# Kernel tuning notes

Measured on AMD Instinct MI355X. Metric: run time of the kernel, lower is better.

## Reference

```python
import jax, jax.numpy as jnp
import numpy as np


def _conv1x1(x, w, b=None):
    # x: (N,C,H,W), w: (O,C) -> (N,O,H,W)
    y = jnp.einsum('nchw,oc->nohw', x, w)
    return y if b is None else y + b[None, :, None, None]


def _norm(f):
    # per-channel zero-mean / unit-std over (N,H,W); torch.std is unbiased (ddof=1)
    mean = f.mean(axis=(0, 2, 3), keepdims=True)
    std = f.std(axis=(0, 2, 3), ddof=1, keepdims=True)
    return (f - mean) / (std + 1e-6)


def _causal_attention(x, w_cls):
    N, C, H, W = x.shape
    M = _conv1x1(x, w_cls).reshape(N, -1, H * W)     # (N,K,HW)
    sm = jax.nn.softmax(M, axis=2)                   # softmax over spatial
    return jnp.einsum('nkp,ncp->nkc', sm, x.reshape(N, C, H * W))  # (N,K,C)


def _ccnet(x, wq, bq, wk, bk, wv, bv, gamma1):
    B, C, H, W = x.shape
    q = _conv1x1(x, wq, bq)  # (B,Cq,H,W)
    k = _conv1x1(x, wk, bk)
    v = _conv1x1(x, wv, bv)  # (B,C,H,W)
    # column (vertical) attention energies with -inf on the self diagonal
    eH = jnp.einsum('bciw,bcjw->biwj', q, k)         # (B,H,W,H)
    eH = jnp.where(jnp.eye(H, dtype=bool)[None, :, None, :], -jnp.inf, eH)
    # row (horizontal) attention energies
    eW = jnp.einsum('bchi,bchj->bhij', q, k)         # (B,H,W,W)
    att = jax.nn.softmax(jnp.concatenate([eH, eW], axis=3), axis=3)
    attH, attW = att[..., :H], att[..., H:]
    outH = jnp.einsum('bcjw,biwj->bciw', v, attH)    # aggregate along column
    outW = jnp.einsum('bchj,bhij->bchi', v, attW)    # aggregate along row
    return gamma1 * (outH + outW) + x


def setup_inputs() -> dict:
    key = jax.random.key(0)
    ks = jax.random.split(key, 10)
    B, C, H, W = 8, 256, 96, 96
    Cq, K = C // 8, 6
    f32 = jnp.float32
    return {
        'preds_S': jax.random.normal(ks[0], (B, C, H, W), f32),
        'preds_T': jax.random.normal(ks[1], (B, C, H, W), f32),
        'w_cls': jax.random.normal(ks[2], (K, C), f32) * 0.05,
        'wq': jax.random.normal(ks[3], (Cq, C), f32) * 0.05,
        'bq': jnp.zeros((Cq,), f32),
        'wk': jax.random.normal(ks[4], (Cq, C), f32) * 0.05,
        'bk': jnp.zeros((Cq,), f32),
        'wv': jax.random.normal(ks[5], (C, C), f32) * 0.05,
        'bv': jnp.zeros((C,), f32),
        'gamma1': jax.random.normal(ks[6], (1,), f32) * 0.1,
    }


def reference(preds_S, preds_T, w_cls, wq, bq, wk, bk, wv, bv, gamma1):
    CA_W, CC_W = 0.0005, 1e-05
    N = preds_S.shape[0]
    s = _norm(preds_S)
    t = _norm(preds_T)
    ca_t = _causal_attention(t, w_cls)
    ca_s = _causal_attention(s, w_cls)
    ca_loss = jnp.sum((ca_t - ca_s) ** 2) / N
    cc_t = _ccnet(t, wq, bq, wk, bk, wv, bv, gamma1)
    cc_s = _ccnet(s, wq, bq, wk, bk, wv, bv, gamma1)
    cc_loss = jnp.sum((cc_t - cc_s) ** 2) / N
    return ca_loss * CA_W + cc_loss * CC_W
```

## Files before the change

### kernel.cpp

```cpp
#include <hip/hip_runtime.h>
#include <math.h>

#define NBAT 8
#define NC   256
#define NH   96
#define NW   96
#define NP   9216
#define NCQ  32
#define NKC  6
#define NL   192
#define NV   320
#define NTOT 73728

typedef __attribute__((ext_vector_type(4))) float  floatx4;
typedef __attribute__((ext_vector_type(8))) short  short8;

__device__ __forceinline__ float bf2f(unsigned short h){
  return __uint_as_float(((unsigned)h) << 16);
}
__device__ __forceinline__ unsigned short f2bf(float f){
  unsigned u = __float_as_uint(f);
  u += 0x7FFFu + ((u >> 16) & 1u);
  return (unsigned short)(u >> 16);
}

union F4 { float4 v; float a[4]; };

__device__ __forceinline__ float warpReduceSum(float v){
  #pragma unroll
  for (int m = 32; m; m >>= 1) v += __shfl_xor(v, m);
  return v;
}
__device__ __forceinline__ float warpReduceMax(float v){
  #pragma unroll
  for (int m = 32; m; m >>= 1) v = fmaxf(v, __shfl_xor(v, m));
  return v;
}
__device__ float blockReduceSum(float v){
  __shared__ float lds[8];
  v = warpReduceSum(v);
  int wid = threadIdx.x >> 6, lane = threadIdx.x & 63;
  int nw = blockDim.x >> 6;
  if (lane == 0) lds[wid] = v;
  __syncthreads();
  if (wid == 0){
    v = (lane < nw) ? lds[lane] : 0.f;
    #pragma unroll
    for (int m = 4; m; m >>= 1) v += __shfl_xor(v, m);
  }
  __syncthreads();
  return v;
}
__device__ float blockReduceMax(float v){
  __shared__ float lds[8];
  v = warpReduceMax(v);
  int wid = threadIdx.x >> 6, lane = threadIdx.x & 63;
  int nw = blockDim.x >> 6;
  if (lane == 0) lds[wid] = v;
  __syncthreads();
  if (wid == 0){
    v = (lane < nw) ? lds[lane] : -INFINITY;
    #pragma unroll
    for (int m = 4; m; m >>= 1) v = fmaxf(v, __shfl_xor(v, m));
  }
  __syncthreads();
  return v;
}

__global__ __launch_bounds__(256)
void k_stats(const float* __restrict__ S, const float* __restrict__ T,
             float* __restrict__ s_sum, float* __restrict__ s_sq){
  int blk = blockIdx.x;
  int t = blk / (NC * NBAT);
  int rem = blk % (NC * NBAT);
  int c = rem / NBAT;
  int n = rem % NBAT;
  const float4* x4 = (const float4*)((t ? T : S) + ((size_t)n * NC + c) * NP);
  float s = 0.f, q = 0.f;
  for (int p = threadIdx.x; p < NP / 4; p += 256){
    F4 f; f.v = x4[p];
    #pragma unroll
    for (int j = 0; j < 4; j++){ s += f.a[j]; q += f.a[j] * f.a[j]; }
  }
  s = blockReduceSum(s);
  q = blockReduceSum(q);
  if (threadIdx.x == 0){
    atomicAdd(&s_sum[t * NC + c], s);
    atomicAdd(&s_sq[t * NC + c], q);
  }
}

__global__ __launch_bounds__(512)
void k_finalize(const float* __restrict__ s_sum, const float* __restrict__ s_sq,
                float* __restrict__ mean, float* __restrict__ inv){
  int i = threadIdx.x;
  if (i < 2 * NC){
    float s = s_sum[i], q = s_sq[i];
    float m = s / (float)NTOT;
    float var = (q - s * m) / (float)(NTOT - 1);
    var = fmaxf(var, 0.f);
    mean[i] = m;
    inv[i] = 1.f / (sqrtf(var) + 1e-6f);
  }
}

__global__ __launch_bounds__(256)
void k_xn(const float* __restrict__ S, const float* __restrict__ T, int b0,
          const float* __restrict__ mean, const float* __restrict__ inv,
          unsigned short* __restrict__ XNT, unsigned short* __restrict__ XNS){
  int pt = blockIdx.x, ct = blockIdx.y;
  int bb = blockIdx.z >> 1, ts = blockIdx.z & 1;
  int t = ts ? 0 : 1;
  const float* x0 = ts ? S : T;
  unsigned short* XN = (ts ? XNS : XNT) + (size_t)bb * NP * NC;
  int bg = b0 + bb;
  int p0 = pt * 64, c0 = ct * 64;
  __shared__ float tile[64 * 65];
  const float* x = x0 + ((size_t)bg * NC + c0) * NP + p0;
  #pragma unroll
  for (int i = 0; i < 4; i++){
    int idx = threadIdx.x + i * 256;
    int r = idx >> 4, g = (idx & 15) * 4;
    F4 f; f.v = *(const float4*)(x + (size_t)r * NP + g);
    float m = mean[t * NC + c0 + r], iv = inv[t * NC + c0 + r];
    #pragma unroll
    for (int j = 0; j < 4; j++) tile[(g + j) * 65 + r] = (f.a[j] - m) * iv;
  }
  __syncthreads();
  #pragma unroll
  for (int i = 0; i < 4; i++){
    int idx = threadIdx.x + i * 256;
    int p = idx >> 4, g = (idx & 15) * 4;
    unsigned lo = (unsigned)f2bf(tile[p * 65 + g + 0]) | ((unsigned)f2bf(tile[p * 65 + g + 1]) << 16);
    unsigned hi = (unsigned)f2bf(tile[p * 65 + g + 2]) | ((unsigned)f2bf(tile[p * 65 + g + 3]) << 16);
    uint2 u; u.x = lo; u.y = hi;
    *(uint2*)(XN + ((size_t)(p0 + p)) * NC + c0 + g) = u;
  }
}

__global__ __launch_bounds__(256)
void k_caM(const unsigned short* __restrict__ XNT, const unsigned short* __restrict__ XNS,
           const float* __restrict__ wcls, int b0,
           float* __restrict__ smca){
  int pt = blockIdx.x, bb = blockIdx.y, ts = blockIdx.z;
  int t = ts ? 0 : 1;
  const unsigned short* XN = (ts ? XNS : XNT) + (size_t)bb * NP * NC;
  __shared__ float wcf[NKC * NC];
  for (int idx = threadIdx.x; idx < NKC * NC; idx += 256) wcf[idx] = wcls[idx];
  __syncthreads();
  int p = pt * 256 + threadIdx.x;
  const unsigned short* row = XN + (size_t)p * NC;
  float acc[NKC];
  #pragma unroll
  for (int k = 0; k < NKC; k++) acc[k] = 0.f;
  for (int c = 0; c < NC; c += 8){
    short8 v = *(const short8*)(row + c);
    #pragma unroll
    for (int j = 0; j < 8; j++){
      float xv = bf2f((unsigned short)v[j]);
      #pragma unroll
      for (int k = 0; k < NKC; k++) acc[k] += wcf[k * NC + c + j] * xv;
    }
  }
  size_t base = ((size_t)(t * NBAT + b0 + bb) * NKC) * NP + p;
  #pragma unroll
  for (int k = 0; k < NKC; k++) smca[base + (size_t)k * NP] = acc[k];
}

__global__ __launch_bounds__(256)
void k_caSoftmax(float* __restrict__ smca, int b0){
  int r = blockIdx.x;
  int bb = r / (2 * NKC);
  int rem = r % (2 * NKC);
  int ts = rem / NKC, k = rem % NKC;
  int t = ts ? 0 : 1;
  float* row = smca + ((size_t)(t * NBAT + b0 + bb) * NKC + k) * NP;
  float m = -INFINITY;
  for (int p = threadIdx.x; p < NP; p += 256) m = fmaxf(m, row[p]);
  m = blockReduceMax(m);
  __shared__ float bm, bs;
  if (threadIdx.x == 0) bm = m;
  __syncthreads();
  m = bm;
  float s = 0.f;
  for (int p = threadIdx.x; p < NP; p += 256) s += expf(row[p] - m);
  s = blockReduceSum(s);
  if (threadIdx.x == 0) bs = 1.f / s;
  __syncthreads();
  float rs = bs;
  for (int p = threadIdx.x; p < NP; p += 256) row[p] = expf(row[p] - m) * rs;
}

__global__ __launch_bounds__(256)
void k_caOut(const unsigned short* __restrict__ XNT, const unsigned short* __restrict__ XNS,
             const float* __restrict__ smca, int b0,
             float* __restrict__ ca){
  int ks = blockIdx.x, bb = blockIdx.y, ts = blockIdx.z;
  int t = ts ? 0 : 1;
  const unsigned short* XN = (ts ? XNS : XNT) + (size_t)bb * NP * NC;
  int p0 = ks * 256;
  __shared__ float smt[NKC * 256];
  const float* smbase = smca + (size_t)(t * NBAT + b0 + bb) * NKC * NP;
  for (int idx = threadIdx.x; idx < NKC * 256; idx += 256){
    int k = idx >> 8, pp = idx & 255;
    smt[idx] = smbase[(size_t)k * NP + p0 + pp];
  }
  __syncthreads();
  int c = threadIdx.x;
  float acc[NKC];
  #pragma unroll
  for (int k = 0; k < NKC; k++) acc[k] = 0.f;
  const unsigned short* xp = XN + (size_t)p0 * NC + c;
  for (int pp = 0; pp < 256; pp++){
    float xv = bf2f(xp[(size_t)pp * NC]);
    #pragma unroll
    for (int k = 0; k < NKC; k++) acc[k] += smt[k * 256 + pp] * xv;
  }
  float* cab = ca + ((size_t)(t * NBAT + b0 + bb) * NKC) * NC + c;
  #pragma unroll
  for (int k = 0; k < NKC; k++) atomicAdd(&cab[(size_t)k * NC], acc[k]);
}

__global__ __launch_bounds__(256)
void k_caLoss(const float* __restrict__ ca, float* __restrict__ out){
  int i = blockIdx.x * 256 + threadIdx.x;
  float d = 0.f;
  if (i < NBAT * NKC * NC) d = ca[(size_t)NBAT * NKC * NC + i] - ca[i];
  float ss = blockReduceSum(d * d);
  if (threadIdx.x == 0) atomicAdd(out, ss * (0.0005f / 8.0f));
}

__global__ __launch_bounds__(256)
void k_wconv(const float* __restrict__ wv, const float* __restrict__ wq,
             const float* __restrict__ wk, unsigned short* __restrict__ Wb){
  int n = blockIdx.x;
  const float* src = (n < 256) ? (wv + (size_t)n * NC)
                   : (n < 288) ? (wq + (size_t)(n - 256) * NC)
                               : (wk + (size_t)(n - 288) * NC);
  Wb[(size_t)n * NC + threadIdx.x] = f2bf(src[threadIdx.x]);
}

__global__ __launch_bounds__(256)
void k_v(const unsigned short* __restrict__ XNT, const unsigned short* __restrict__ XNS,
         const unsigned short* __restrict__ Wb,
         const float* __restrict__ bv, const float* __restrict__ bq,
         const float* __restrict__ bk,
         unsigned short* __restrict__ VT1T, unsigned short* __restrict__ VT1S,
         unsigned short* __restrict__ qT, unsigned short* __restrict__ kT,
         unsigned short* __restrict__ qS, unsigned short* __restrict__ kS){
  int pt = blockIdx.x;
  int bb = blockIdx.y >> 1, ts = blockIdx.y & 1;
  const unsigned short* XN = (ts ? XNS : XNT) + (size_t)bb * NP * NC;
  unsigned short* VT1 = (ts ? VT1S : VT1T) + (size_t)bb * NP * NC;
  unsigned short* qb  = (ts ? qS : qT) + (size_t)bb * NP * NCQ;
  unsigned short* kb  = (ts ? kS : kT) + (size_t)bb * NP * NCQ;
  int p0 = pt * 64;
  __shared__ unsigned short Wl[NV * 40];
  int lane = threadIdx.x & 63;
  int wid = threadIdx.x >> 6;
  int col = lane & 15, quad = lane >> 4;
  const unsigned short* xnb = XN + (size_t)(p0 + wid * 16 + col) * NC;
  floatx4 acc[20];
  #pragma unroll
  for (int nt = 0; nt < 20; nt++) acc[nt] = (floatx4){0.f, 0.f, 0.f, 0.f};

  int ci_n[5], ci_k8[5];
  #pragma unroll
  for (int i = 0; i < 5; i++){ int ci = i * 256 + threadIdx.x; ci_n[i] = ci >> 2; ci_k8[i] = (ci & 3) * 8; }

  short8 w[5];
  #pragma unroll
  for (int i = 0; i < 5; i++)
    w[i] = *(const short8*)(Wb + (size_t)ci_n[i] * NC + ci_k8[i]);

  for (int ks = 0; ks < 8; ks++){
    if (ks) __syncthreads();
    #pragma unroll
    for (int i = 0; i < 5; i++)
      *(short8*)(Wl + ci_n[i] * 40 + ci_k8[i]) = w[i];
    __syncthreads();
    if (ks < 7){
      int k0n = (ks + 1) * 32;
      #pragma unroll
      for (int i = 0; i < 5; i++)
        w[i] = *(const short8*)(Wb + (size_t)ci_n[i] * NC + k0n + ci_k8[i]);
    }
    short8 a = *(const short8*)(xnb + ks * 32 + quad * 8);
    #pragma unroll
    for (int nt = 0; nt < 20; nt++){
      short8 b = *(const short8*)(Wl + (nt * 16 + col) * 40 + quad * 8);
      acc[nt] = __builtin_amdgcn_mfma_f32_16x16x32_bf16(a, b, acc[nt], 0, 0, 0);
    }
  }

  int prow0 = p0 + wid * 16 + quad * 4;
  #pragma unroll
  for (int nt = 0; nt < 16; nt++){
    int c = nt * 16 + col;
    float bias = bv[c];
    uint2 u;
    u.x = (unsigned)f2bf(acc[nt][0] + bias) | ((unsigned)f2bf(acc[nt][1] + bias) << 16);
    u.y = (unsigned)f2bf(acc[nt][2] + bias) | ((unsigned)f2bf(acc[nt][3] + bias) << 16);
    *(uint2*)(VT1 + (size_t)c * NP + prow0) = u;
  }
  #pragma unroll
  for (int nt = 16; nt < 18; nt++){
    int c = (nt - 16) * 16 + col;
    float bias = bq[c];
    #pragma unroll
    for (int i = 0; i < 4; i++)
      qb[((size_t)(prow0 + i)) * NCQ + c] = f2bf(acc[nt][i] + bias);
  }
  #pragma unroll
  for (int nt = 18; nt < 20; nt++){
    int c = (nt - 18) * 16 + col;
    float bias = bk[c];
    #pragma unroll
    for (int i = 0; i < 4; i++)
      kb[((size_t)(prow0 + i)) * NCQ + c] = f2bf(acc[nt][i] + bias);
  }
}

__global__ __launch_bounds__(256)
void k_vt(const unsigned short* __restrict__ VT1T, const unsigned short* __restrict__ VT1S,
          unsigned short* __restrict__ VT2T, unsigned short* __restrict__ VT2S){
  int c = blockIdx.x;
  int bb = blockIdx.y >> 1, ts = blockIdx.y & 1;
  const unsigned short* VT1 = (ts ? VT1S : VT1T) + (size_t)bb * NP * NC;
  unsigned short* VT2 = (ts ? VT2S : VT2T) + (size_t)bb * NP * NC;
  __shared__ unsigned short tile[96 * 104];
  size_t base = (size_t)c * NP;
  for (int idx = threadIdx.x; idx < 1152; idx += 256){
    int h = idx / 12, g = idx % 12;
    short8 v = *(const short8*)(VT1 + base + h * 96 + g * 8);
    #pragma unroll
    for (int kk = 0; kk < 8; kk++) tile[(g * 8 + kk) * 104 + h] = ((unsigned short*)&v)[kk];
  }
  __syncthreads();
  for (int idx = threadIdx.x; idx < 1152; idx += 256){
    int w = idx / 12, g = idx % 12;
    short8 v = *(const short8*)(tile + w * 104 + g * 8);
    *(short8*)(VT2 + base + w * 96 + g * 8) = v;
  }
}

__global__ __launch_bounds__(256)
void k_e(const unsigned short* __restrict__ qT, const unsigned short* __restrict__ kT,
         const unsigned short* __restrict__ qS, const unsigned short* __restrict__ kS,
         unsigned short* __restrict__ attT, unsigned short* __restrict__ attS){
  int x = blockIdx.x, which = blockIdx.z;
  int bb = blockIdx.y >> 1, ts = blockIdx.y & 1;
  const unsigned short* qb = (ts ? qS : qT) + (size_t)bb * NP * NCQ;
  const unsigned short* kb = (ts ? kS : kT) + (size_t)bb * NP * NCQ;
  unsigned short* att = (ts ? attS : attT) + (size_t)bb * NP * NL;
  int lane = threadIdx.x & 63, wid = threadIdx.x >> 6;
  int col = lane & 15, quad = lane >> 4;
  int mi0 = (wid & 1) * 3, ni0 = (wid >> 1) * 3;
  short8 a[3], b[3];
  if (which == 0){
    #pragma unroll
    for (int m = 0; m < 3; m++)
      a[m] = *(const short8*)(qb + ((size_t)(((mi0 + m) * 16 + col) * 96 + x)) * NCQ + quad * 8);
    #pragma unroll
    for (int n = 0; n < 3; n++)
      b[n] = *(const short8*)(kb + ((size_t)(((ni0 + n) * 16 + col) * 96 + x)) * NCQ + quad * 8);
  } else {
    #pragma unroll
    for (int m = 0; m < 3; m++)
      a[m] = *(const short8*)(qb + ((size_t)(x * 96 + (mi0 + m) * 16 + col)) * NCQ + quad * 8);
    #pragma unroll
    for (int n = 0; n < 3; n++)
      b[n] = *(const short8*)(kb + ((size_t)(x * 96 + (ni0 + n) * 16 + col)) * NCQ + quad * 8);
  }
  floatx4 acc[3][3];
  #pragma unroll
  for (int m = 0; m < 3; m++)
    #pragma unroll
    for (int n = 0; n < 3; n++){
      acc[m][n] = (floatx4){0.f, 0.f, 0.f, 0.f};
      acc[m][n] = __builtin_amdgcn_mfma_f32_16x16x32_bf16(a[m], b[n], acc[m][n], 0, 0, 0);
    }
  #pragma unroll
  for (int m = 0; m < 3; m++)
    #pragma unroll
    for (int n = 0; n < 3; n++){
      int j = (ni0 + n) * 16 + col;
      #pragma unroll
      for (int r = 0; r < 4; r++){
        int i = (mi0 + m) * 16 + quad * 4 + r;
        int p = which ? (x * 96 + i) : (i * 96 + x);
        float v = (!which && j == i) ? -INFINITY : acc[m][n][r];
        att[(size_t)p * NL + (which ? 96 + j : j)] = f2bf(v);
      }
    }
}

__global__ __launch_bounds__(256)
void k_attSoftmax(unsigned short* __restrict__ attT, unsigned short* __restrict__ attS,
                  int nbp){
  int q = blockIdx.x * 4 + (threadIdx.x >> 6);
  int lane = threadIdx.x & 63;
  unsigned short* row = (q < nbp) ? (attT + (size_t)q * NL)
                                  : (attS + (size_t)(q - nbp) * NL);
  float e0 = bf2f(row[lane]);
  float e1 = bf2f(row[64 + lane]);
  float e2 = bf2f(row[128 + lane]);
  float m = fmaxf(e0, fmaxf(e1, e2));
  m = warpReduceMax(m);
  float x0 = expf(e0 - m), x1 = expf(e1 - m), x2 = expf(e2 - m);
  float s = warpReduceSum(x0 + x1 + x2);
  float rs = 1.f / s;
  row[lane]       = f2bf(x0 * rs);
  row[64 + lane]  = f2bf(x1 * rs);
  row[128 + lane] = f2bf(x2 * rs);
}

__global__ __launch_bounds__(256)
void k_outH(const unsigned short* __restrict__ VT2T, const unsigned short* __restrict__ VT2S,
            const unsigned short* __restrict__ attT, const unsigned short* __restrict__ attS,
            unsigned short* __restrict__ OHT, unsigned short* __restrict__ OHS){
  int w = blockIdx.x, cs = blockIdx.z;
  int bb = blockIdx.y >> 1, ts = blockIdx.y & 1;
  const unsigned short* VT2 = (ts ? VT2S : VT2T) + (size_t)bb * NP * NC;
  const unsigned short* att = (ts ? attS : attT) + (size_t)bb * NP * NL;
  unsigned short* OH = (ts ? OHS : OHT) + (size_t)bb * NP * NC;
  int lane = threadIdx.x & 63, wid = threadIdx.x >> 6;
  int col = lane & 15, quad = lane >> 4;
  int c = cs * 64 + wid * 16 + col;
  floatx4 acc[6];
  #pragma unroll
  for (int m = 0; m < 6; m++) acc[m] = (floatx4){0.f, 0.f, 0.f, 0.f};
  #pragma unroll
  for (int ks = 0; ks < 3; ks++){
    int k0 = ks * 32 + quad * 8;
    short8 a[6], b;
    #pragma unroll
    for (int m = 0; m < 6; m++)
      a[m] = *(const short8*)(att + ((size_t)((m * 16 + col) * 96 + w)) * NL + k0);
    b = *(const short8*)(VT2 + (size_t)c * NP + w * 96 + k0);
    #pragma unroll
    for (int m = 0; m < 6; m++)
      acc[m] = __builtin_amdgcn_mfma_f32_16x16x32_bf16(a[m], b, acc[m], 0, 0, 0);
  }
  #pragma unroll
  for (int m = 0; m < 6; m++){
    #pragma unroll
    for (int r = 0; r < 4; r++){
      int i = m * 16 + quad * 4 + r;
      OH[((size_t)(i * 96 + w)) * NC + c] = f2bf(acc[m][r]);
    }
  }
}

__global__ __launch_bounds__(256)
void k_outWL(const unsigned short* __restrict__ VT1T, const unsigned short* __restrict__ attT,
             const unsigned short* __restrict__ OHT,
             const unsigned short* __restrict__ VT1S, const unsigned short* __restrict__ attS,
             const unsigned short* __restrict__ OHS,
             const unsigned short* __restrict__ XNT, const unsigned short* __restrict__ XNS,
             const float* __restrict__ gamma,
             float* __restrict__ out){
  int h = blockIdx.x, bb = blockIdx.y, cs = blockIdx.z;
  size_t pb = (size_t)bb * NP * NC;
  int lane = threadIdx.x & 63, wid = threadIdx.x >> 6;
  int col = lane & 15, quad = lane >> 4;
  int cl = wid * 16 + col;
  int c  = cs * 64 + cl;

  __shared__ unsigned short ohTl[96 * 72];
  __shared__ unsigned short ohSl[96 * 72];
  __shared__ unsigned short dnl [96 * 72];

  #pragma unroll
  for (int k = 0; k < 3; k++){
    int g = threadIdx.x + k * 256;
    int i = g >> 3, cc = (g & 7) * 8;
    size_t ga = pb + ((size_t)(h * 96 + i)) * NC + cs * 64 + cc;
    short8 ot = *(const short8*)(OHT + ga);
    short8 os = *(const short8*)(OHS + ga);
    short8 xt = *(const short8*)(XNT + ga);
    short8 xs = *(const short8*)(XNS + ga);
    short8 dn;
    #pragma unroll
    for (int j = 0; j < 8; j++)
      ((unsigned short*)&dn)[j] = f2bf(bf2f((unsigned short)xt[j]) - bf2f((unsigned short)xs[j]));
    *(short8*)(ohTl + i * 72 + cc) = ot;
    *(short8*)(ohSl + i * 72 + cc) = os;
    *(short8*)(dnl  + i * 72 + cc) = dn;
  }
  __syncthreads();

  floatx4 accT[6], accS[6];
  #pragma unroll
  for (int m = 0; m < 6; m++){
    accT[m] = (floatx4){0.f, 0.f, 0.f, 0.f};
    accS[m] = (floatx4){0.f, 0.f, 0.f, 0.f};
  }
  #pragma unroll
  for (int ks = 0; ks < 3; ks++){
    int k0 = ks * 32 + quad * 8;
    short8 a[6], b;
    #pragma unroll
    for (int m = 0; m < 6; m++)
      a[m] = *(const short8*)(attT + (size_t)bb * NP * NL + ((size_t)(h * 96 + m * 16 + col)) * NL + 96 + k0);
    b = *(const short8*)(VT1T + pb + (size_t)c * NP + h * 96 + k0);
    #pragma unroll
    for (int m = 0; m < 6; m++)
      accT[m] = __builtin_amdgcn_mfma_f32_16x16x32_bf16(a[m], b, accT[m], 0, 0, 0);
  }
  #pragma unroll
  for (int ks = 0; ks < 3; ks++){
    int k0 = ks * 32 + quad * 8;
    short8 a[6], b;
    #pragma unroll
    for (int m = 0; m < 6; m++)
      a[m] = *(const short8*)(attS + (size_t)bb * NP * NL + ((size_t)(h * 96 + m * 16 + col)) * NL + 96 + k0);
    b = *(const short8*)(VT1S + pb + (size_t)c * NP + h * 96 + k0);
    #pragma unroll
    for (int m = 0; m < 6; m++)
      accS[m] = __builtin_amdgcn_mfma_f32_16x16x32_bf16(a[m], b, accS[m], 0, 0, 0);
  }

  float g = gamma[0];
  float ss = 0.f;
  #pragma unroll
  for (int m = 0; m < 6; m++){
    int i0 = m * 16 + quad * 4;
    #pragma unroll
    for (int r = 0; r < 4; r++){
      int i = i0 + r;
      float oT = accT[m][r] + bf2f(ohTl[i * 72 + cl]);
      float oS = accS[m][r] + bf2f(ohSl[i * 72 + cl]);
      float d = g * (oT - oS) + bf2f(dnl[i * 72 + cl]);
      ss += d * d;
    }
  }
  ss = blockReduceSum(ss);
  if (threadIdx.x == 0) atomicAdd(out, ss * (1e-5f / 8.0f));
}

extern "C" void kernel_launch(void* const* d_in, const int* in_sizes, int n_in,
                              void* d_out, int out_size, void* d_ws, size_t ws_size,
                              hipStream_t stream){
  (void)in_sizes; (void)n_in; (void)out_size;
  const float* S    = (const float*)d_in[0];
  const float* T    = (const float*)d_in[1];
  const float* wcls = (const float*)d_in[2];
  const float* wq   = (const float*)d_in[3];
  const float* bq   = (const float*)d_in[4];
  const float* wk   = (const float*)d_in[5];
  const float* bk   = (const float*)d_in[6];
  const float* wv   = (const float*)d_in[7];
  const float* bv   = (const float*)d_in[8];
  const float* gamma= (const float*)d_in[9];
  float* out = (float*)d_out;

  char* base = (char*)d_ws;
  size_t off = 0;
  auto alloc = [&](size_t b){ size_t o = off; off += (b + 255) & ~(size_t)255; return o; };
  size_t o_ssum = alloc(2 * NC * 4);
  size_t o_ssq  = alloc(2 * NC * 4);
  size_t o_mean = alloc(2 * NC * 4);
  size_t o_inv  = alloc(2 * NC * 4);
  size_t o_wb   = alloc((size_t)NV * NC * 2);
  size_t o_ca   = alloc((size_t)2 * NBAT * NKC * NC * 4);
  size_t o_smca = alloc((size_t)2 * NBAT * NKC * NP * 4);
  size_t fixed = off;

  const size_t PB  = (size_t)NP * NC * 2;
  const size_t ATT = (size_t)NP * NL * 2;
  const size_t QB  = (size_t)NP * NCQ * 2;
  size_t per_b = 8 * PB + 2 * ATT + 4 * QB;
  int NB = 8;
  while (NB > 1 && fixed + (size_t)NB * per_b + 8192 > ws_size) NB >>= 1;

  size_t o_xnT = alloc((size_t)NB * PB);
  size_t o_xnS = alloc((size_t)NB * PB);
  size_t o_v1T = alloc((size_t)NB * PB);
  size_t o_v1S = alloc((size_t)NB * PB);
  size_t o_v2T = alloc((size_t)NB * PB);
  size_t o_v2S = alloc((size_t)NB * PB);
  size_t o_ohT = alloc((size_t)NB * PB);
  size_t o_ohS = alloc((size_t)NB * PB);
  size_t o_aT  = alloc((size_t)NB * ATT);
  size_t o_aS  = alloc((size_t)NB * ATT);
  size_t o_qT  = alloc((size_t)NB * QB);
  size_t o_kT  = alloc((size_t)NB * QB);
  size_t o_qS  = alloc((size_t)NB * QB);
  size_t o_kS  = alloc((size_t)NB * QB);

  float* ssum = (float*)(base + o_ssum);
  float* ssq  = (float*)(base + o_ssq);
  float* mean = (float*)(base + o_mean);
  float* inv  = (float*)(base + o_inv);
  float* ca   = (float*)(base + o_ca);
  float* smca = (float*)(base + o_smca);
  unsigned short* Wb  = (unsigned short*)(base + o_wb);
  unsigned short* XNT = (unsigned short*)(base + o_xnT);
  unsigned short* XNS = (unsigned short*)(base + o_xnS);
  unsigned short* V1T = (unsigned short*)(base + o_v1T);
  unsigned short* V1S = (unsigned short*)(base + o_v1S);
  unsigned short* V2T = (unsigned short*)(base + o_v2T);
  unsigned short* V2S = (unsigned short*)(base + o_v2S);
  unsigned short* OHT = (unsigned short*)(base + o_ohT);
  unsigned short* OHS = (unsigned short*)(base + o_ohS);
  unsigned short* attT= (unsigned short*)(base + o_aT);
  unsigned short* attS= (unsigned short*)(base + o_aS);
  unsigned short* qT  = (unsigned short*)(base + o_qT);
  unsigned short* kT  = (unsigned short*)(base + o_kT);
  unsigned short* qS  = (unsigned short*)(base + o_qS);
  unsigned short* kS  = (unsigned short*)(base + o_kS);

  hipMemsetAsync(d_out, 0, 4, stream);
  hipMemsetAsync(base + o_ssum, 0, 4096, stream);
  hipMemsetAsync(base + o_ca, 0, (size_t)2 * NBAT * NKC * NC * 4, stream);

  k_stats<<<dim3(2 * NC * NBAT), 256, 0, stream>>>(S, T, ssum, ssq);
  k_finalize<<<1, 512, 0, stream>>>(ssum, ssq, mean, inv);
  k_wconv<<<dim3(NV), 256, 0, stream>>>(wv, wq, wk, Wb);

  for (int b0 = 0; b0 < NBAT; b0 += NB){
    k_xn<<<dim3(144, 4, 2 * NB), 256, 0, stream>>>(S, T, b0, mean, inv, XNT, XNS);
    k_caM<<<dim3(36, NB, 2), 256, 0, stream>>>(XNT, XNS, wcls, b0, smca);
    k_caSoftmax<<<dim3(2 * NB * NKC), 256, 0, stream>>>(smca, b0);
    k_caOut<<<dim3(36, NB, 2), 256, 0, stream>>>(XNT, XNS, smca, b0, ca);
    k_v<<<dim3(144, 2 * NB), 256, 0, stream>>>(XNT, XNS, Wb, bv, bq, bk,
                                               V1T, V1S, qT, kT, qS, kS);
    k_vt<<<dim3(256, 2 * NB), 256, 0, stream>>>(V1T, V1S, V2T, V2S);
    k_e<<<dim3(96, 2 * NB, 2), 256, 0, stream>>>(qT, kT, qS, kS, attT, attS);
    k_attSoftmax<<<dim3(2 * NB * NP / 4), 256, 0, stream>>>(attT, attS, NB * NP);
    k_outH<<<dim3(96, 2 * NB, 4), 256, 0, stream>>>(V2T, V2S, attT, attS, OHT, OHS);
    k_outWL<<<dim3(96, NB, 4), 256, 0, stream>>>(V1T, attT, OHT, V1S, attS, OHS,
                                                 XNT, XNS, gamma, out);
  }
  k_caLoss<<<dim3(48), 256, 0, stream>>>(ca, out);
}
```

Before: 647.5 us.

## Relayout V, attention and OH buffers into row-blocked contiguous tiles

The V projection is now stored as [h][c][w] (and the transposed copy as [w][c][h]), so each row or column tile used by the aggregation kernels is contiguous. The concatenated 192-wide attention rows are split into separate H (stored transposed) and W buffers, and OH is written channel-slice-major so k_outWL reads contiguous blocks. k_stats also loads all nine float4 per thread up front instead of in a loop, to expose more memory-level parallelism. The aim is better coalescing and locality across the attention pipeline, at the cost of strided softmax access to the transposed H rows and more index arithmetic.

```diff
diff --git a/kernel.cpp b/kernel.cpp
--- a/kernel.cpp
+++ b/kernel.cpp
@@ -8,7 +8,6 @@
 #define NP   9216
 #define NCQ  32
 #define NKC  6
-#define NL   192
 #define NV   320
 #define NTOT 73728
 
@@ -76,12 +75,14 @@
   int c = rem / NBAT;
   int n = rem % NBAT;
   const float4* x4 = (const float4*)((t ? T : S) + ((size_t)n * NC + c) * NP);
+  F4 f[9];
+  #pragma unroll
+  for (int j = 0; j < 9; j++) f[j].v = x4[threadIdx.x + j * 256];
   float s = 0.f, q = 0.f;
-  for (int p = threadIdx.x; p < NP / 4; p += 256){
-    F4 f; f.v = x4[p];
-    #pragma unroll
-    for (int j = 0; j < 4; j++){ s += f.a[j]; q += f.a[j] * f.a[j]; }
-  }
+  #pragma unroll
+  for (int j = 0; j < 9; j++)
+    #pragma unroll
+    for (int e = 0; e < 4; e++){ s += f[j].a[e]; q += f[j].a[e] * f[j].a[e]; }
   s = blockReduceSum(s);
   q = blockReduceSum(q);
   if (threadIdx.x == 0){
@@ -245,13 +246,13 @@
          const unsigned short* __restrict__ Wb,
          const float* __restrict__ bv, const float* __restrict__ bq,
          const float* __restrict__ bk,
-         unsigned short* __restrict__ VT1T, unsigned short* __restrict__ VT1S,
+         unsigned short* __restrict__ V1T, unsigned short* __restrict__ V1S,
          unsigned short* __restrict__ qT, unsigned short* __restrict__ kT,
          unsigned short* __restrict__ qS, unsigned short* __restrict__ kS){
   int pt = blockIdx.x;
   int bb = blockIdx.y >> 1, ts = blockIdx.y & 1;
   const unsigned short* XN = (ts ? XNS : XNT) + (size_t)bb * NP * NC;
-  unsigned short* VT1 = (ts ? VT1S : VT1T) + (size_t)bb * NP * NC;
+  unsigned short* V1 = (ts ? V1S : V1T) + (size_t)bb * NP * NC;
   unsigned short* qb  = (ts ? qS : qT) + (size_t)bb * NP * NCQ;
   unsigned short* kb  = (ts ? kS : kT) + (size_t)bb * NP * NCQ;
   int p0 = pt * 64;
@@ -294,6 +295,7 @@
   }
 
   int prow0 = p0 + wid * 16 + quad * 4;
+  int hh = prow0 / 96, ww = prow0 % 96;
   #pragma unroll
   for (int nt = 0; nt < 16; nt++){
     int c = nt * 16 + col;
@@ -301,7 +303,7 @@
     uint2 u;
     u.x = (unsigned)f2bf(acc[nt][0] + bias) | ((unsigned)f2bf(acc[nt][1] + bias) << 16);
     u.y = (unsigned)f2bf(acc[nt][2] + bias) | ((unsigned)f2bf(acc[nt][3] + bias) << 16);
-    *(uint2*)(VT1 + (size_t)c * NP + prow0) = u;
+    *(uint2*)(V1 + ((size_t)(hh * 256 + c)) * 96 + ww) = u;
   }
   #pragma unroll
   for (int nt = 16; nt < 18; nt++){
@@ -322,37 +324,46 @@
 }
 
 __global__ __launch_bounds__(256)
-void k_vt(const unsigned short* __restrict__ VT1T, const unsigned short* __restrict__ VT1S,
-          unsigned short* __restrict__ VT2T, unsigned short* __restrict__ VT2S){
-  int c = blockIdx.x;
+void k_vt(const unsigned short* __restrict__ V1T, const unsigned short* __restrict__ V1S,
+          unsigned short* __restrict__ V2T, unsigned short* __restrict__ V2S){
+  int cp = blockIdx.x;
   int bb = blockIdx.y >> 1, ts = blockIdx.y & 1;
-  const unsigned short* VT1 = (ts ? VT1S : VT1T) + (size_t)bb * NP * NC;
-  unsigned short* VT2 = (ts ? VT2S : VT2T) + (size_t)bb * NP * NC;
-  __shared__ unsigned short tile[96 * 104];
-  size_t base = (size_t)c * NP;
-  for (int idx = threadIdx.x; idx < 1152; idx += 256){
-    int h = idx / 12, g = idx % 12;
-    short8 v = *(const short8*)(VT1 + base + h * 96 + g * 8);
-    #pragma unroll
-    for (int kk = 0; kk < 8; kk++) tile[(g * 8 + kk) * 104 + h] = ((unsigned short*)&v)[kk];
-  }
-  __syncthreads();
-  for (int idx = threadIdx.x; idx < 1152; idx += 256){
-    int w = idx / 12, g = idx % 12;
-    short8 v = *(const short8*)(tile + w * 104 + g * 8);
-    *(short8*)(VT2 + base + w * 96 + g * 8) = v;
+  const unsigned short* V1 = (ts ? V1S : V1T) + (size_t)bb * NP * NC;
+  unsigned short* V2 = (ts ? V2S : V2T) + (size_t)bb * NP * NC;
+  int c0 = cp * 2;
+  __shared__ unsigned short tile[2 * 96 * 104];
+  #pragma unroll
+  for (int k = 0; k < 9; k++){
+    int idx = threadIdx.x + k * 256;
+    int cl = idx / 1152, rem = idx % 1152;
+    int h = rem / 12, g = rem % 12;
+    short8 v = *(const short8*)(V1 + ((size_t)(h * 256 + c0 + cl)) * 96 + g * 8);
+    #pragma unroll
+    for (int jj = 0; jj < 8; jj++)
+      tile[cl * 9984 + (g * 8 + jj) * 104 + h] = ((unsigned short*)&v)[jj];
+  }
+  __syncthreads();
+  #pragma unroll
+  for (int k = 0; k < 9; k++){
+    int idx = threadIdx.x + k * 256;
+    int cl = idx / 1152, rem = idx % 1152;
+    int w = rem / 12, g = rem % 12;
+    short8 v = *(const short8*)(tile + cl * 9984 + w * 104 + g * 8);
+    *(short8*)(V2 + ((size_t)(w * 256 + c0 + cl)) * 96 + g * 8) = v;
   }
 }
 
 __global__ __launch_bounds__(256)
 void k_e(const unsigned short* __restrict__ qT, const unsigned short* __restrict__ kT,
          const unsigned short* __restrict__ qS, const unsigned short* __restrict__ kS,
-         unsigned short* __restrict__ attT, unsigned short* __restrict__ attS){
+         unsigned short* __restrict__ attHtT, unsigned short* __restrict__ attWT,
+         unsigned short* __restrict__ attHtS, unsigned short* __restrict__ attWS){
   int x = blockIdx.x, which = blockIdx.z;
   int bb = blockIdx.y >> 1, ts = blockIdx.y & 1;
   const unsigned short* qb = (ts ? qS : qT) + (size_t)bb * NP * NCQ;
   const unsigned short* kb = (ts ? kS : kT) + (size_t)bb * NP * NCQ;
-  unsigned short* att = (ts ? attS : attT) + (size_t)bb * NP * NL;
+  unsigned short* att = (which ? (ts ? attWS : attWT) : (ts ? attHtS : attHtT))
+                        + (size_t)bb * NP * 96;
   int lane = threadIdx.x & 63, wid = threadIdx.x >> 6;
   int col = lane & 15, quad = lane >> 4;
   int mi0 = (wid & 1) * 3, ni0 = (wid >> 1) * 3;
@@ -388,45 +399,57 @@
       #pragma unroll
       for (int r = 0; r < 4; r++){
         int i = (mi0 + m) * 16 + quad * 4 + r;
-        int p = which ? (x * 96 + i) : (i * 96 + x);
         float v = (!which && j == i) ? -INFINITY : acc[m][n][r];
-        att[(size_t)p * NL + (which ? 96 + j : j)] = f2bf(v);
+        att[((size_t)(x * 96 + i)) * 96 + j] = f2bf(v);
       }
     }
 }
 
 __global__ __launch_bounds__(256)
-void k_attSoftmax(unsigned short* __restrict__ attT, unsigned short* __restrict__ attS,
+void k_attSoftmax(unsigned short* __restrict__ attHtT, unsigned short* __restrict__ attWT,
+                  unsigned short* __restrict__ attHtS, unsigned short* __restrict__ attWS,
                   int nbp){
   int q = blockIdx.x * 4 + (threadIdx.x >> 6);
   int lane = threadIdx.x & 63;
-  unsigned short* row = (q < nbp) ? (attT + (size_t)q * NL)
-                                  : (attS + (size_t)(q - nbp) * NL);
-  float e0 = bf2f(row[lane]);
-  float e1 = bf2f(row[64 + lane]);
-  float e2 = bf2f(row[128 + lane]);
-  float m = fmaxf(e0, fmaxf(e1, e2));
+  int sS = (q >= nbp);
+  int ql = sS ? q - nbp : q;
+  unsigned short* aHt = sS ? attHtS : attHtT;
+  unsigned short* aW  = sS ? attWS  : attWT;
+  int bb = ql / NP, p = ql % NP;
+  unsigned short* rowW = aW  + ((size_t)(bb * NP + p)) * 96;
+  unsigned short* rowH = aHt + ((size_t)(bb * NP + (p % 96) * 96 + p / 96)) * 96;
+  float h0 = bf2f(rowH[lane]);
+  float w0 = bf2f(rowW[lane]);
+  float h1 = (lane < 32) ? bf2f(rowH[64 + lane]) : -INFINITY;
+  float w1 = (lane < 32) ? bf2f(rowW[64 + lane]) : -INFINITY;
+  float m = fmaxf(fmaxf(h0, h1), fmaxf(w0, w1));
   m = warpReduceMax(m);
-  float x0 = expf(e0 - m), x1 = expf(e1 - m), x2 = expf(e2 - m);
-  float s = warpReduceSum(x0 + x1 + x2);
+  float xh0 = expf(h0 - m), xw0 = expf(w0 - m);
+  float xh1 = (lane < 32) ? expf(h1 - m) : 0.f;
+  float xw1 = (lane < 32) ? expf(w1 - m) : 0.f;
+  float s = warpReduceSum(xh0 + xw0 + xh1 + xw1);
   float rs = 1.f / s;
-  row[lane]       = f2bf(x0 * rs);
-  row[64 + lane]  = f2bf(x1 * rs);
-  row[128 + lane] = f2bf(x2 * rs);
-}
-
-__global__ __launch_bounds__(256)
-void k_outH(const unsigned short* __restrict__ VT2T, const unsigned short* __restrict__ VT2S,
-            const unsigned short* __restrict__ attT, const unsigned short* __restrict__ attS,
+  rowH[lane] = f2bf(xh0 * rs);
+  rowW[lane] = f2bf(xw0 * rs);
+  if (lane < 32){
+    rowH[64 + lane] = f2bf(xh1 * rs);
+    rowW[64 + lane] = f2bf(xw1 * rs);
+  }
+}
+
+__global__ __launch_bounds__(256)
+void k_outH(const unsigned short* __restrict__ V2T, const unsigned short* __restrict__ V2S,
+            const unsigned short* __restrict__ attHtT, const unsigned short* __restrict__ attHtS,
             unsigned short* __restrict__ OHT, unsigned short* __restrict__ OHS){
   int w = blockIdx.x, cs = blockIdx.z;
   int bb = blockIdx.y >> 1, ts = blockIdx.y & 1;
-  const unsigned short* VT2 = (ts ? VT2S : VT2T) + (size_t)bb * NP * NC;
-  const unsigned short* att = (ts ? attS : attT) + (size_t)bb * NP * NL;
-  unsigned short* OH = (ts ? OHS : OHT) + (size_t)bb * NP * NC;
+  const unsigned short* V2 = (ts ? V2S : V2T) + (size_t)bb * NP * NC;
+  const unsigned short* att = (ts ? attHtS : attHtT) + (size_t)bb * NP * 96;
+  unsigned short* OH = (ts ? OHS : OHT) + (size_t)bb * NP * NC + (size_t)cs * NP * 64;
   int lane = threadIdx.x & 63, wid = threadIdx.x >> 6;
   int col = lane & 15, quad = lane >> 4;
-  int c = cs * 64 + wid * 16 + col;
+  int cl = wid * 16 + col;
+  int c = cs * 64 + cl;
   floatx4 acc[6];
   #pragma unroll
   for (int m = 0; m < 6; m++) acc[m] = (floatx4){0.f, 0.f, 0.f, 0.f};
@@ -436,8 +459,8 @@
     short8 a[6], b;
     #pragma unroll
     for (int m = 0; m < 6; m++)
-      a[m] = *(const short8*)(att + ((size_t)((m * 16 + col) * 96 + w)) * NL + k0);
-    b = *(const short8*)(VT2 + (size_t)c * NP + w * 96 + k0);
+      a[m] = *(const short8*)(att + ((size_t)(w * 96 + m * 16 + col)) * 96 + k0);
+    b = *(const short8*)(V2 + ((size_t)(w * 256 + c)) * 96 + k0);
     #pragma unroll
     for (int m = 0; m < 6; m++)
       acc[m] = __builtin_amdgcn_mfma_f32_16x16x32_bf16(a[m], b, acc[m], 0, 0, 0);
@@ -447,15 +470,15 @@
     #pragma unroll
     for (int r = 0; r < 4; r++){
       int i = m * 16 + quad * 4 + r;
-      OH[((size_t)(i * 96 + w)) * NC + c] = f2bf(acc[m][r]);
+      OH[((size_t)(i * 96 + w)) * 64 + cl] = f2bf(acc[m][r]);
     }
   }
 }
 
 __global__ __launch_bounds__(256)
-void k_outWL(const unsigned short* __restrict__ VT1T, const unsigned short* __restrict__ attT,
+void k_outWL(const unsigned short* __restrict__ V1T, const unsigned short* __restrict__ attWT,
              const unsigned short* __restrict__ OHT,
-             const unsigned short* __restrict__ VT1S, const unsigned short* __restrict__ attS,
+             const unsigned short* __restrict__ V1S, const unsigned short* __restrict__ attWS,
              const unsigned short* __restrict__ OHS,
              const unsigned short* __restrict__ XNT, const unsigned short* __restrict__ XNS,
              const float* __restrict__ gamma,
@@ -471,15 +494,17 @@
   __shared__ unsigned short ohSl[96 * 72];
   __shared__ unsigned short dnl [96 * 72];
 
+  const unsigned short* OHTb = OHT + pb + (size_t)cs * NP * 64 + (size_t)(h * 96) * 64;
+  const unsigned short* OHSb = OHS + pb + (size_t)cs * NP * 64 + (size_t)(h * 96) * 64;
   #pragma unroll
   for (int k = 0; k < 3; k++){
     int g = threadIdx.x + k * 256;
     int i = g >> 3, cc = (g & 7) * 8;
-    size_t ga = pb + ((size_t)(h * 96 + i)) * NC + cs * 64 + cc;
-    short8 ot = *(const short8*)(OHT + ga);
-    short8 os = *(const short8*)(OHS + ga);
-    short8 xt = *(const short8*)(XNT + ga);
-    short8 xs = *(const short8*)(XNS + ga);
+    short8 ot = *(const short8*)(OHTb + g * 8);
+    short8 os = *(const short8*)(OHSb + g * 8);
+    size_t gx = pb + ((size_t)(h * 96 + i)) * NC + cs * 64 + cc;
+    short8 xt = *(const short8*)(XNT + gx);
+    short8 xs = *(const short8*)(XNS + gx);
     short8 dn;
     #pragma unroll
     for (int j = 0; j < 8; j++)
@@ -502,8 +527,8 @@
     short8 a[6], b;
     #pragma unroll
     for (int m = 0; m < 6; m++)
-      a[m] = *(const short8*)(attT + (size_t)bb * NP * NL + ((size_t)(h * 96 + m * 16 + col)) * NL + 96 + k0);
-    b = *(const short8*)(VT1T + pb + (size_t)c * NP + h * 96 + k0);
+      a[m] = *(const short8*)(attWT + (size_t)bb * NP * 96 + ((size_t)(h * 96 + m * 16 + col)) * 96 + k0);
+    b = *(const short8*)(V1T + pb + ((size_t)(h * 256 + c)) * 96 + k0);
     #pragma unroll
     for (int m = 0; m < 6; m++)
       accT[m] = __builtin_amdgcn_mfma_f32_16x16x32_bf16(a[m], b, accT[m], 0, 0, 0);
@@ -514,8 +539,8 @@
     short8 a[6], b;
     #pragma unroll
     for (int m = 0; m < 6; m++)
-      a[m] = *(const short8*)(attS + (size_t)bb * NP * NL + ((size_t)(h * 96 + m * 16 + col)) * NL + 96 + k0);
-    b = *(const short8*)(VT1S + pb + (size_t)c * NP + h * 96 + k0);
+      a[m] = *(const short8*)(attWS + (size_t)bb * NP * 96 + ((size_t)(h * 96 + m * 16 + col)) * 96 + k0);
+    b = *(const short8*)(V1S + pb + ((size_t)(h * 256 + c)) * 96 + k0);
     #pragma unroll
     for (int m = 0; m < 6; m++)
       accS[m] = __builtin_amdgcn_mfma_f32_16x16x32_bf16(a[m], b, accS[m], 0, 0, 0);
@@ -568,9 +593,9 @@
   size_t fixed = off;
 
   const size_t PB  = (size_t)NP * NC * 2;
-  const size_t ATT = (size_t)NP * NL * 2;
+  const size_t AT1 = (size_t)NP * 96 * 2;
   const size_t QB  = (size_t)NP * NCQ * 2;
-  size_t per_b = 8 * PB + 2 * ATT + 4 * QB;
+  size_t per_b = 8 * PB + 4 * AT1 + 4 * QB;
   int NB = 8;
   while (NB > 1 && fixed + (size_t)NB * per_b + 8192 > ws_size) NB >>= 1;
 
@@ -582,8 +607,10 @@
   size_t o_v2S = alloc((size_t)NB * PB);
   size_t o_ohT = alloc((size_t)NB * PB);
   size_t o_ohS = alloc((size_t)NB * PB);
-  size_t o_aT  = alloc((size_t)NB * ATT);
-  size_t o_aS  = alloc((size_t)NB * ATT);
+  size_t o_hT  = alloc((size_t)NB * AT1);
+  size_t o_wT  = alloc((size_t)NB * AT1);
+  size_t o_hS  = alloc((size_t)NB * AT1);
+  size_t o_wS  = alloc((size_t)NB * AT1);
   size_t o_qT  = alloc((size_t)NB * QB);
   size_t o_kT  = alloc((size_t)NB * QB);
   size_t o_qS  = alloc((size_t)NB * QB);
@@ -595,21 +622,23 @@
   float* inv  = (float*)(base + o_inv);
   float* ca   = (float*)(base + o_ca);
   float* smca = (float*)(base + o_smca);
-  unsigned short* Wb  = (unsigned short*)(base + o_wb);
-  unsigned short* XNT = (unsigned short*)(base + o_xnT);
-  unsigned short* XNS = (unsigned short*)(base + o_xnS);
-  unsigned short* V1T = (unsigned short*)(base + o_v1T);
-  unsigned short* V1S = (unsigned short*)(base + o_v1S);
-  unsigned short* V2T = (unsigned short*)(base + o_v2T);
-  unsigned short* V2S = (unsigned short*)(base + o_v2S);
-  unsigned short* OHT = (unsigned short*)(base + o_ohT);
-  unsigned short* OHS = (unsigned short*)(base + o_ohS);
-  unsigned short* attT= (unsigned short*)(base + o_aT);
-  unsigned short* attS= (unsigned short*)(base + o_aS);
-  unsigned short* qT  = (unsigned short*)(base + o_qT);
-  unsigned short* kT  = (unsigned short*)(base + o_kT);
-  unsigned short* qS  = (unsigned short*)(base + o_qS);
-  unsigned short* kS  = (unsigned short*)(base + o_kS);
+  unsigned short* Wb   = (unsigned short*)(base + o_wb);
+  unsigned short* XNT  = (unsigned short*)(base + o_xnT);
+  unsigned short* XNS  = (unsigned short*)(base + o_xnS);
+  unsigned short* V1T  = (unsigned short*)(base + o_v1T);
+  unsigned short* V1S  = (unsigned short*)(base + o_v1S);
+  unsigned short* V2T  = (unsigned short*)(base + o_v2T);
+  unsigned short* V2S  = (unsigned short*)(base + o_v2S);
+  unsigned short* OHT  = (unsigned short*)(base + o_ohT);
+  unsigned short* OHS  = (unsigned short*)(base + o_ohS);
+  unsigned short* aHtT = (unsigned short*)(base + o_hT);
+  unsigned short* aWT  = (unsigned short*)(base + o_wT);
+  unsigned short* aHtS = (unsigned short*)(base + o_hS);
+  unsigned short* aWS  = (unsigned short*)(base + o_wS);
+  unsigned short* qT   = (unsigned short*)(base + o_qT);
+  unsigned short* kT   = (unsigned short*)(base + o_kT);
+  unsigned short* qS   = (unsigned short*)(base + o_qS);
+  unsigned short* kS   = (unsigned short*)(base + o_kS);
 
   hipMemsetAsync(d_out, 0, 4, stream);
   hipMemsetAsync(base + o_ssum, 0, 4096, stream);
@@ -626,11 +655,11 @@
     k_caOut<<<dim3(36, NB, 2), 256, 0, stream>>>(XNT, XNS, smca, b0, ca);
     k_v<<<dim3(144, 2 * NB), 256, 0, stream>>>(XNT, XNS, Wb, bv, bq, bk,
                                                V1T, V1S, qT, kT, qS, kS);
-    k_vt<<<dim3(256, 2 * NB), 256, 0, stream>>>(V1T, V1S, V2T, V2S);
-    k_e<<<dim3(96, 2 * NB, 2), 256, 0, stream>>>(qT, kT, qS, kS, attT, attS);
-    k_attSoftmax<<<dim3(2 * NB * NP / 4), 256, 0, stream>>>(attT, attS, NB * NP);
-    k_outH<<<dim3(96, 2 * NB, 4), 256, 0, stream>>>(V2T, V2S, attT, attS, OHT, OHS);
-    k_outWL<<<dim3(96, NB, 4), 256, 0, stream>>>(V1T, attT, OHT, V1S, attS, OHS,
+    k_vt<<<dim3(128, 2 * NB), 256, 0, stream>>>(V1T, V1S, V2T, V2S);
+    k_e<<<dim3(96, 2 * NB, 2), 256, 0, stream>>>(qT, kT, qS, kS, aHtT, aWT, aHtS, aWS);
+    k_attSoftmax<<<dim3(2 * NB * NP / 4), 256, 0, stream>>>(aHtT, aWT, aHtS, aWS, NB * NP);
+    k_outH<<<dim3(96, 2 * NB, 4), 256, 0, stream>>>(V2T, V2S, aHtT, aHtS, OHT, OHS);
+    k_outWL<<<dim3(96, NB, 4), 256, 0, stream>>>(V1T, aWT, OHT, V1S, aWS, OHS,
                                                  XNT, XNS, gamma, out);
   }
   k_caLoss<<<dim3(48), 256, 0, stream>>>(ca, out);
```

Result: faster. 611.1 us (-5.6%).
